# Optimization experiments

Hardware: AMD Instinct MI355X
Metric: run time of the kernel (lower is better)

The kernel has to match this reference:

```python
import jax, jax.numpy as jnp
import numpy as np

NUM_HEADS = 12
EPS = 1e-6


def _rms_norm(x, w):
    # RMSNorm over the full channel dim (applied before head split), fp32 math
    return x * jax.lax.rsqrt(jnp.mean(x * x, axis=-1, keepdims=True) + EPS) * w


def _rope_apply(t, F, H, W, freqs):
    # t: [B, S, n, d] with S == F*H*W; freqs: [1024, d//2] angles
    B, S, n, d = t.shape
    c = d // 2
    s0 = c - 2 * (c // 3)  # temporal split (22 when d=128)
    s1 = c // 3            # spatial splits (21, 21)
    f0, f1, f2 = freqs[:, :s0], freqs[:, s0:s0 + s1], freqs[:, s0 + s1:]
    ang = jnp.concatenate([
        jnp.broadcast_to(f0[:F, None, None, :], (F, H, W, s0)),
        jnp.broadcast_to(f1[None, :H, None, :], (F, H, W, s1)),
        jnp.broadcast_to(f2[None, None, :W, :], (F, H, W, s1)),
    ], axis=-1).reshape(S, c)                      # [S, c]
    cos = jnp.cos(ang)[None, :, None, :]           # [1, S, 1, c]
    sin = jnp.sin(ang)[None, :, None, :]
    tp = t.reshape(B, S, n, c, 2)
    te, to = tp[..., 0], tp[..., 1]                # complex (real, imag) pairs
    rot = jnp.stack([te * cos - to * sin, te * sin + to * cos], axis=-1)
    return rot.reshape(B, S, n, d)


def reference(x, seq_lens, grid_sizes, freqs, Wq, bq, Wk, bk, Wv, bv, Wo, bo, norm_q_w, norm_k_w):
    B, S, C = x.shape
    n = NUM_HEADS
    d = C // n
    gs = np.asarray(grid_sizes)[0]
    F, H, W = int(gs[0]), int(gs[1]), int(gs[2])  # static: L == F*H*W, same per sample

    q = _rms_norm(x @ Wq.T + bq, norm_q_w).reshape(B, S, n, d)
    k = _rms_norm(x @ Wk.T + bk, norm_k_w).reshape(B, S, n, d)
    v = (x @ Wv.T + bv).reshape(B, S, n, d)

    q = _rope_apply(q, F, H, W, freqs)
    k = _rope_apply(k, F, H, W, freqs)

    scale = 1.0 / jnp.sqrt(jnp.float32(d))
    scores = jnp.einsum('bqnd,bknd->bnqk', q, k) * scale   # [B, n, S, S]
    kmask = jnp.arange(S)[None, :] < seq_lens[:, None]      # [B, S] valid keys
    scores = jnp.where(kmask[:, None, None, :], scores, -jnp.inf)
    attn = jax.nn.softmax(scores, axis=-1)
    out = jnp.einsum('bnqk,bknd->bqnd', attn, v).reshape(B, S, C)
    return out @ Wo.T + bo


def setup_inputs() -> dict:
    key = jax.random.key(0)
    ks = jax.random.split(key, 10)
    B, F, H, W = 2, 4, 24, 32
    S = F * H * W  # 3072
    C = 1536
    d = C // NUM_HEADS  # 128
    c = d // 2          # 64

    x = jax.random.normal(ks[0], (B, S, C), dtype=jnp.float32)
    seq_lens = jnp.array([S, 2500], dtype=jnp.int32)
    grid_sizes = jnp.array([[F, H, W]] * B, dtype=jnp.int32)

    # rope angles: outer(pos, 1/theta^(2i/dim)) per split [22, 21, 21]
    def rope_params(max_len, dim_k, theta=10000.0):
        inv = 1.0 / (theta ** (np.arange(0, dim_k, 2, dtype=np.float64) / dim_k))
        return np.outer(np.arange(max_len), inv)
    s0 = c - 2 * (c // 3)
    s1 = c // 3
    freqs = jnp.asarray(np.concatenate([
        rope_params(1024, 2 * s0), rope_params(1024, 2 * s1), rope_params(1024, 2 * s1)
    ], axis=1), dtype=jnp.float32)  # [1024, 64]

    std = 0.02
    def lin(k):
        return jax.random.normal(k, (C, C), dtype=jnp.float32) * std
    return {
        'x': x, 'seq_lens': seq_lens, 'grid_sizes': grid_sizes, 'freqs': freqs,
        'Wq': lin(ks[1]), 'bq': jnp.zeros((C,), jnp.float32),
        'Wk': lin(ks[2]), 'bk': jnp.zeros((C,), jnp.float32),
        'Wv': lin(ks[3]), 'bv': jnp.zeros((C,), jnp.float32),
        'Wo': lin(ks[4]), 'bo': jnp.zeros((C,), jnp.float32),
        'norm_q_w': jnp.ones((C,), jnp.float32),
        'norm_k_w': jnp.ones((C,), jnp.float32),
    }
```

## Files before the change

### kernel.cpp

```cpp
#include <hip/hip_runtime.h>
#include <hip/hip_bf16.h>
#include <math.h>

#define NB 2
#define SS 3072
#define CC 1536
#define NH 12
#define DH 128
#define NTOK (NB * SS)
#define WE (CC * CC)
#define LOG2E 1.4426950408889634f

typedef __attribute__((ext_vector_type(8))) short short8;
typedef __attribute__((ext_vector_type(4))) float floatx4;

#define GLOAD(g, l) __builtin_amdgcn_global_load_lds( \
    (const __attribute__((address_space(1))) void*)(g), \
    (__attribute__((address_space(3))) void*)(l), 16, 0, 0)

__device__ __forceinline__ unsigned short f2bf(float f) {
    unsigned u = __float_as_uint(f);
    u += 0x7fffu + ((u >> 16) & 1u);
    return (unsigned short)(u >> 16);
}
__device__ __forceinline__ int swz(int row, int q) {
    return row * 4 + (q ^ ((row >> 1) & 3));
}

__global__ __launch_bounds__(256) void cast_all(
    const float* __restrict__ x,
    const float* __restrict__ w0, const float* __restrict__ w1,
    const float* __restrict__ w2, const float* __restrict__ w3,
    unsigned short* __restrict__ o)
{
    const int y = blockIdx.y;
    const float* src = (y < 4) ? x + (size_t)y * WE
                     : (y == 4) ? w0 : (y == 5) ? w1 : (y == 6) ? w2 : w3;
    size_t i = ((size_t)blockIdx.x * 256 + threadIdx.x) * 4;
    float4 v = *(const float4*)&src[i];
    uint2 u;
    u.x = (unsigned)f2bf(v.x) | ((unsigned)f2bf(v.y) << 16);
    u.y = (unsigned)f2bf(v.z) | ((unsigned)f2bf(v.w) << 16);
    *(uint2*)&o[(size_t)y * WE + i] = u;
}

__global__ __launch_bounds__(256) void rope_table(
    const float* __restrict__ freqs, const int* __restrict__ gsz,
    float2* __restrict__ tab)
{
    const int id = blockIdx.x * 256 + threadIdx.x;
    const int s = id >> 6, pj = id & 63;
    const int Hg = gsz[1], Wg = gsz[2];
    const int f = s / (Hg * Wg);
    const int rem = s - f * Hg * Wg;
    const int hh = rem / Wg;
    const int ww = rem - hh * Wg;
    const int row = (pj < 22) ? f : ((pj < 43) ? hh : ww);
    float sn, cs;
    sincosf(freqs[row * 64 + pj], &sn, &cs);
    tab[id] = make_float2(cs, sn);
}

__global__ __launch_bounds__(256) void qkv_gemm(
    const unsigned short* __restrict__ X,
    const unsigned short* __restrict__ Wqb, const unsigned short* __restrict__ Wkb,
    const unsigned short* __restrict__ Wvb,
    const float* __restrict__ bq, const float* __restrict__ bk,
    const float* __restrict__ bv,
    unsigned short* __restrict__ qo, unsigned short* __restrict__ ko,
    unsigned short* __restrict__ vto)
{
    __shared__ unsigned short As[128 * 32];
    __shared__ unsigned short Bs[128 * 32];
    const int tid = threadIdx.x;
    const int w = tid >> 6, l = tid & 63;
    const int jseg = blockIdx.y / 12;
    const unsigned short* Wt = (jseg == 0) ? Wqb : (jseg == 1) ? Wkb : Wvb;
    const float* bias        = (jseg == 0) ? bq  : (jseg == 1) ? bk  : bv;
    unsigned short* Y        = (jseg == 0) ? qo  : (jseg == 1) ? ko  : vto;
    const int i0 = blockIdx.x * 128, j0 = (blockIdx.y % 12) * 128;
    const int srow = tid >> 2;
    const int gk8 = (((tid & 3) ^ ((srow >> 1) & 3))) * 8;

    floatx4 acc[4][4] = {};
    for (int k0 = 0; k0 < CC; k0 += 32) {
        __syncthreads();
        GLOAD(X + (size_t)(i0 + srow) * CC + k0 + gk8,        As + (size_t)tid * 8);
        GLOAD(X + (size_t)(i0 + 64 + srow) * CC + k0 + gk8,   As + (size_t)(256 + tid) * 8);
        GLOAD(Wt + (size_t)(j0 + srow) * CC + k0 + gk8,       Bs + (size_t)tid * 8);
        GLOAD(Wt + (size_t)(j0 + 64 + srow) * CC + k0 + gk8,  Bs + (size_t)(256 + tid) * 8);
        __syncthreads();
        const int wr = (w >> 1) * 64, wc = (w & 1) * 64;
        short8 af[4], bf[4];
        #pragma unroll
        for (int mb = 0; mb < 4; ++mb)
            af[mb] = *(const short8*)&As[swz(wr + mb * 16 + (l & 15), l >> 4) * 8];
        #pragma unroll
        for (int nb = 0; nb < 4; ++nb)
            bf[nb] = *(const short8*)&Bs[swz(wc + nb * 16 + (l & 15), l >> 4) * 8];
        #pragma unroll
        for (int mb = 0; mb < 4; ++mb)
            #pragma unroll
            for (int nb = 0; nb < 4; ++nb)
                acc[mb][nb] = __builtin_amdgcn_mfma_f32_16x16x32_bf16(
                    af[mb], bf[nb], acc[mb][nb], 0, 0, 0);
    }

    const int wr = (w >> 1) * 64, wc = (w & 1) * 64;
    #pragma unroll
    for (int mb = 0; mb < 4; ++mb)
        #pragma unroll
        for (int nb = 0; nb < 4; ++nb) {
            const int n = j0 + wc + nb * 16 + (l & 15);
            const float bv2 = bias[n];
            const int h = n >> 7, td = n & 127;
            #pragma unroll
            for (int r = 0; r < 4; ++r) {
                const int m = i0 + wr + mb * 16 + (l >> 4) * 4 + r;
                const float val = acc[mb][nb][r] + bv2;
                const int b = (m >= SS) ? 1 : 0;
                const int s = m - b * SS;
                if (jseg < 2)
                    Y[((size_t)(b * NH + h) * SS + s) * DH + td] = f2bf(val);
                else
                    Y[((size_t)(b * NH + h) * DH + td) * SS + s] = f2bf(val);
            }
        }
}

__global__ __launch_bounds__(256) void gemm_o(
    const unsigned short* __restrict__ X, const unsigned short* __restrict__ Wt,
    const float* __restrict__ bias, float* __restrict__ Y)
{
    __shared__ unsigned short As[128 * 32];
    __shared__ unsigned short Bs[128 * 32];
    const int tid = threadIdx.x;
    const int w = tid >> 6, l = tid & 63;
    const int i0 = blockIdx.x * 128, j0 = blockIdx.y * 128;
    const int srow = tid >> 2;
    const int gk8 = (((tid & 3) ^ ((srow >> 1) & 3))) * 8;

    floatx4 acc[4][4] = {};
    for (int k0 = 0; k0 < CC; k0 += 32) {
        __syncthreads();
        GLOAD(X + (size_t)(i0 + srow) * CC + k0 + gk8,        As + (size_t)tid * 8);
        GLOAD(X + (size_t)(i0 + 64 + srow) * CC + k0 + gk8,   As + (size_t)(256 + tid) * 8);
        GLOAD(Wt + (size_t)(j0 + srow) * CC + k0 + gk8,       Bs + (size_t)tid * 8);
        GLOAD(Wt + (size_t)(j0 + 64 + srow) * CC + k0 + gk8,  Bs + (size_t)(256 + tid) * 8);
        __syncthreads();
        const int wr = (w >> 1) * 64, wc = (w & 1) * 64;
        short8 af[4], bf[4];
        #pragma unroll
        for (int mb = 0; mb < 4; ++mb)
            af[mb] = *(const short8*)&As[swz(wr + mb * 16 + (l & 15), l >> 4) * 8];
        #pragma unroll
        for (int nb = 0; nb < 4; ++nb)
            bf[nb] = *(const short8*)&Bs[swz(wc + nb * 16 + (l & 15), l >> 4) * 8];
        #pragma unroll
        for (int mb = 0; mb < 4; ++mb)
            #pragma unroll
            for (int nb = 0; nb < 4; ++nb)
                acc[mb][nb] = __builtin_amdgcn_mfma_f32_16x16x32_bf16(
                    af[mb], bf[nb], acc[mb][nb], 0, 0, 0);
    }

    const int wr = (w >> 1) * 64, wc = (w & 1) * 64;
    #pragma unroll
    for (int mb = 0; mb < 4; ++mb)
        #pragma unroll
        for (int nb = 0; nb < 4; ++nb) {
            const int n = j0 + wc + nb * 16 + (l & 15);
            const float bv = bias[n];
            #pragma unroll
            for (int r = 0; r < 4; ++r) {
                const int m = i0 + wr + mb * 16 + (l >> 4) * 4 + r;
                Y[(size_t)m * CC + n] = acc[mb][nb][r] + bv;
            }
        }
}

__global__ __launch_bounds__(256) void norm_rope(
    unsigned short* __restrict__ qb, unsigned short* __restrict__ kb,
    const float* __restrict__ nqw, const float* __restrict__ nkw,
    const float2* __restrict__ tab)
{
    const int bid = blockIdx.x;
    const int which = (bid >= NTOK) ? 1 : 0;
    const int tok = bid - which * NTOK;
    unsigned short* t    = which ? kb : qb;
    const float* wgt     = which ? nkw : nqw;
    const float outscale = which ? 1.0f : 0.08838834764831845f * LOG2E;
    const int b = tok / SS, s = tok - b * SS;
    const int tid = threadIdx.x;

    float2 vals[3];
    size_t addrs[3];
    float ss = 0.f;
    #pragma unroll
    for (int kt = 0; kt < 3; ++kt) {
        int p = tid + kt * 256;
        int h = p >> 6, pj = p & 63;
        size_t addr = ((size_t)(b * NH + h) * SS + s) * DH + 2 * pj;
        addrs[kt] = addr;
        unsigned u = *(const unsigned*)&t[addr];
        float2 v;
        v.x = __uint_as_float(u << 16);
        v.y = __uint_as_float(u & 0xffff0000u);
        vals[kt] = v;
        ss += v.x * v.x + v.y * v.y;
    }
    #pragma unroll
    for (int off = 32; off > 0; off >>= 1) ss += __shfl_down(ss, off, 64);
    __shared__ float red[4];
    if ((tid & 63) == 0) red[tid >> 6] = ss;
    __syncthreads();
    const float total = red[0] + red[1] + red[2] + red[3];
    const float rstd = rsqrtf(total * (1.0f / CC) + 1e-6f) * outscale;

    #pragma unroll
    for (int kt = 0; kt < 3; ++kt) {
        int p = tid + kt * 256;
        int h = p >> 6, pj = p & 63;
        float2 cssn = tab[s * 64 + pj];
        int ch = h * DH + 2 * pj;
        float te = vals[kt].x * rstd * wgt[ch];
        float to = vals[kt].y * rstd * wgt[ch + 1];
        unsigned o = (unsigned)f2bf(te * cssn.x - to * cssn.y) |
                     ((unsigned)f2bf(te * cssn.y + to * cssn.x) << 16);
        *(unsigned*)&t[addrs[kt]] = o;
    }
}

__global__ __launch_bounds__(256, 2) void flash_attn_mfma(
    const unsigned short* __restrict__ qg, const unsigned short* __restrict__ kg,
    const unsigned short* __restrict__ vg, const int* __restrict__ seq_lens,
    unsigned short* __restrict__ out)
{
    __shared__ unsigned short lds[32768];
    const int tid = threadIdx.x;
    const int w = tid >> 6, l = tid & 63;

    const int bid = blockIdx.x;
    const int qt = bid / (NB * NH);
    const int rem0 = bid - qt * (NB * NH);
    const int h = rem0 >> 1;
    const int b = rem0 & 1;
    const int slen = seq_lens[b];
    const int s0 = qt * 128;

    const unsigned short* qbase = qg + ((size_t)(b * NH + h) * SS + s0) * DH;
    const unsigned short* kbase = kg + ((size_t)(b * NH + h) * SS) * DH;
    const unsigned short* vbase = vg + ((size_t)(b * NH + h) * DH) * SS;

    #pragma unroll
    for (int i = 0; i < 8; ++i) {
        int cid = i * 256 + tid;
        int kc = cid >> 9, r2 = cid & 511, row = r2 >> 2, sq = r2 & 3;
        GLOAD(qbase + (size_t)row * DH + kc * 32 + (sq ^ ((row >> 1) & 3)) * 8,
              lds + (size_t)cid * 8);
    }
    __syncthreads();
    short8 qf[2][4];
    #pragma unroll
    for (int rb = 0; rb < 2; ++rb)
        #pragma unroll
        for (int kc = 0; kc < 4; ++kc)
            qf[rb][kc] = *(const short8*)&lds[(kc * 512 + swz(w * 32 + rb * 16 + (l & 15), l >> 4)) * 8];
    __syncthreads();

    int ksrc[4], vsrc[4];
    #pragma unroll
    for (int i = 0; i < 4; ++i) {
        int cid = i * 256 + tid;
        {   int kc = cid >> 8, r2 = cid & 255, row = r2 >> 2, sq = r2 & 3;
            ksrc[i] = row * DH + kc * 32 + (sq ^ ((row >> 1) & 3)) * 8; }
        {   int ks = cid >> 9, r2 = cid & 511, dc = r2 >> 2, sq = r2 & 3;
            vsrc[i] = dc * SS + ks * 32 + (sq ^ ((dc >> 1) & 3)) * 8; }
    }

    const int ntiles = (slen + 63) >> 6;

    #pragma unroll
    for (int i = 0; i < 4; ++i) {
        int cid = i * 256 + tid;
        GLOAD(kbase + ksrc[i],        lds + (size_t)cid * 8);
        GLOAD(vbase + vsrc[i],        lds + 8192 + (size_t)cid * 8);
    }

    floatx4 acc[2][8] = {};
    float lsum[2] = {};
    const int g4 = (l >> 4) * 4;

    for (int kt = 0; kt < ntiles; ++kt) {
        __syncthreads();

        if (kt + 1 < ntiles) {
            const unsigned short* kb2 = kbase + (size_t)(kt + 1) * 64 * DH;
            const unsigned short* vb2 = vbase + (size_t)(kt + 1) * 64;
            unsigned short* dst = lds + ((kt + 1) & 1) * 16384;
            #pragma unroll
            for (int i = 0; i < 4; ++i) {
                int cid = i * 256 + tid;
                GLOAD(kb2 + ksrc[i], dst + (size_t)cid * 8);
                GLOAD(vb2 + vsrc[i], dst + 8192 + (size_t)cid * 8);
            }
        }

        const unsigned short* Ks = lds + (kt & 1) * 16384;
        const unsigned short* Vs = Ks + 8192;

        floatx4 sv[2][4] = {};
        __builtin_amdgcn_s_setprio(1);
        #pragma unroll
        for (int kc = 0; kc < 4; ++kc) {
            short8 kf[4];
            #pragma unroll
            for (int nb = 0; nb < 4; ++nb)
                kf[nb] = *(const short8*)&Ks[(kc * 256 + swz(nb * 16 + (l & 15), l >> 4)) * 8];
            #pragma unroll
            for (int rb = 0; rb < 2; ++rb)
                #pragma unroll
                for (int nb = 0; nb < 4; ++nb)
                    sv[rb][nb] = __builtin_amdgcn_mfma_f32_16x16x32_bf16(
                        kf[nb], qf[rb][kc], sv[rb][nb], 0, 0, 0);
        }
        __builtin_amdgcn_s_setprio(0);

        const int valid = slen - kt * 64;
        short8 pa[2][2];
        #pragma unroll
        for (int rb = 0; rb < 2; ++rb) {
            if (valid >= 64) {
                #pragma unroll
                for (int nb = 0; nb < 4; ++nb)
                    #pragma unroll
                    for (int r = 0; r < 4; ++r)
                        sv[rb][nb][r] = exp2f(sv[rb][nb][r]);
            } else {
                #pragma unroll
                for (int nb = 0; nb < 4; ++nb)
                    #pragma unroll
                    for (int r = 0; r < 4; ++r) {
                        const int key = g4 + r + 16 * nb;
                        sv[rb][nb][r] = (key < valid) ? exp2f(sv[rb][nb][r]) : 0.0f;
                    }
            }
            #pragma unroll
            for (int nb = 0; nb < 4; ++nb)
                lsum[rb] += (sv[rb][nb][0] + sv[rb][nb][1]) +
                            (sv[rb][nb][2] + sv[rb][nb][3]);

            unsigned dw0[4], dw1[4];
            #pragma unroll
            for (int nb = 0; nb < 4; ++nb) {
                union { __hip_bfloat162 v; unsigned u; } c0, c1;
                c0.v = __float22bfloat162_rn(make_float2(sv[rb][nb][0], sv[rb][nb][1]));
                c1.v = __float22bfloat162_rn(make_float2(sv[rb][nb][2], sv[rb][nb][3]));
                dw0[nb] = c0.u;
                dw1[nb] = c1.u;
            }
            #pragma unroll
            for (int ks = 0; ks < 2; ++ks) {
                unsigned x0 = dw0[2 * ks], y0 = dw0[2 * ks + 1];
                unsigned x1 = dw1[2 * ks], y1 = dw1[2 * ks + 1];
                asm("v_permlane32_swap_b32 %0, %1" : "+v"(x0), "+v"(y0));
                asm("v_permlane16_swap_b32 %0, %1" : "+v"(x0), "+v"(y0));
                asm("v_permlane32_swap_b32 %0, %1" : "+v"(x1), "+v"(y1));
                asm("v_permlane16_swap_b32 %0, %1" : "+v"(x1), "+v"(y1));
                union { short8 s; unsigned u[4]; } pk;
                pk.u[0] = x0; pk.u[1] = x1; pk.u[2] = y0; pk.u[3] = y1;
                pa[rb][ks] = pk.s;
            }
        }

        __builtin_amdgcn_s_setprio(1);
        #pragma unroll
        for (int ks = 0; ks < 2; ++ks)
            #pragma unroll
            for (int nb2 = 0; nb2 < 8; ++nb2) {
                short8 vf = *(const short8*)&Vs[(ks * 512 + swz(nb2 * 16 + (l & 15), l >> 4)) * 8];
                #pragma unroll
                for (int rb = 0; rb < 2; ++rb)
                    acc[rb][nb2] = __builtin_amdgcn_mfma_f32_16x16x32_bf16(
                        pa[rb][ks], vf, acc[rb][nb2], 0, 0, 0);
            }
        __builtin_amdgcn_s_setprio(0);
    }

    #pragma unroll
    for (int rb = 0; rb < 2; ++rb) {
        float s = lsum[rb];
        s += __shfl_xor(s, 16, 64);
        s += __shfl_xor(s, 32, 64);
        float rl[4];
        #pragma unroll
        for (int r = 0; r < 4; ++r)
            rl[r] = 1.0f / __shfl(s, g4 + r, 64);
        #pragma unroll
        for (int nb2 = 0; nb2 < 8; ++nb2) {
            const int col = h * DH + nb2 * 16 + (l & 15);
            #pragma unroll
            for (int r = 0; r < 4; ++r) {
                const int srow = s0 + w * 32 + rb * 16 + (l >> 4) * 4 + r;
                out[((size_t)b * SS + srow) * CC + col] = f2bf(acc[rb][nb2][r] * rl[r]);
            }
        }
    }
}

extern "C" void kernel_launch(void* const* d_in, const int* in_sizes, int n_in,
                              void* d_out, int out_size, void* d_ws, size_t ws_size,
                              hipStream_t stream) {
    const float* x          = (const float*)d_in[0];
    const int*   seq_lens   = (const int*)d_in[1];
    const int*   grid_sizes = (const int*)d_in[2];
    const float* freqs      = (const float*)d_in[3];
    const float* Wq         = (const float*)d_in[4];
    const float* bq         = (const float*)d_in[5];
    const float* Wk         = (const float*)d_in[6];
    const float* bk         = (const float*)d_in[7];
    const float* Wv         = (const float*)d_in[8];
    const float* bv         = (const float*)d_in[9];
    const float* Wo         = (const float*)d_in[10];
    const float* bo         = (const float*)d_in[11];
    const float* nqw        = (const float*)d_in[12];
    const float* nkw        = (const float*)d_in[13];
    float* out = (float*)d_out;

    const size_t TE = (size_t)NTOK * CC;
    unsigned short* xb  = (unsigned short*)d_ws;
    unsigned short* wqb = xb + TE;
    unsigned short* wkb = wqb + WE;
    unsigned short* wvb = wkb + WE;
    unsigned short* wob = wvb + WE;
    unsigned short* qb  = wob + WE;
    unsigned short* kb  = qb + TE;
    unsigned short* vtb = kb + TE;
    unsigned short* ab  = vtb + TE;
    float2* tab = (float2*)(ab + TE);

    cast_all<<<dim3(WE / 1024, 8), 256, 0, stream>>>(x, Wq, Wk, Wv, Wo, xb);
    rope_table<<<dim3(SS * 64 / 256), 256, 0, stream>>>(freqs, grid_sizes, tab);

    qkv_gemm<<<dim3(NTOK / 128, 36), 256, 0, stream>>>(
        xb, wqb, wkb, wvb, bq, bk, bv, qb, kb, vtb);

    norm_rope<<<dim3(2 * NTOK), 256, 0, stream>>>(qb, kb, nqw, nkw, tab);

    flash_attn_mfma<<<dim3(NB * NH * (SS / 128)), 256, 0, stream>>>(qb, kb, vtb, seq_lens, ab);

    gemm_o<<<dim3(NTOK / 128, CC / 128), 256, 0, stream>>>(ab, wob, bo, out);
}
```

Baseline: 519.1 us.

## Make flash attention persistent with XCD-aware work queues for L2 locality

The attention kernel becomes persistent with 512 blocks. Each block reads its XCD id and pulls work items from one of eight atomic counters, one per XCD. A table assigns (batch, head) combos to XCDs so that all query tiles sharing the same K/V stay on one XCD's L2, and the table mixes long and short sequences to balance load. Blocks steal from other XCD queues when their own is empty. The counters are zeroed inside rope_table, and the scheme adds atomic and barrier overhead per work item.

```diff
diff --git a/kernel.cpp b/kernel.cpp
--- a/kernel.cpp
+++ b/kernel.cpp
@@ -26,6 +26,11 @@
 __device__ __forceinline__ int swz(int row, int q) {
     return row * 4 + (q ^ ((row >> 1) & 3));
 }
+
+__device__ const int comboTab[24] = {
+    0, 16, 9,   2, 18, 11,   4, 20, 13,   6, 22, 15,
+    8, 1, 17,   10, 3, 19,   12, 5, 21,   14, 7, 23
+};
 
 __global__ __launch_bounds__(256) void cast_all(
     const float* __restrict__ x,
@@ -46,9 +51,10 @@
 
 __global__ __launch_bounds__(256) void rope_table(
     const float* __restrict__ freqs, const int* __restrict__ gsz,
-    float2* __restrict__ tab)
+    float2* __restrict__ tab, int* __restrict__ ctr)
 {
     const int id = blockIdx.x * 256 + threadIdx.x;
+    if (id < 8) ctr[id] = 0;
     const int s = id >> 6, pj = id & 63;
     const int Hg = gsz[1], Wg = gsz[2];
     const int f = s / (Hg * Wg);
@@ -234,39 +240,17 @@
 __global__ __launch_bounds__(256, 2) void flash_attn_mfma(
     const unsigned short* __restrict__ qg, const unsigned short* __restrict__ kg,
     const unsigned short* __restrict__ vg, const int* __restrict__ seq_lens,
-    unsigned short* __restrict__ out)
+    unsigned short* __restrict__ out, int* __restrict__ ctr)
 {
     __shared__ unsigned short lds[32768];
+    __shared__ int sw;
     const int tid = threadIdx.x;
     const int w = tid >> 6, l = tid & 63;
-
-    const int bid = blockIdx.x;
-    const int qt = bid / (NB * NH);
-    const int rem0 = bid - qt * (NB * NH);
-    const int h = rem0 >> 1;
-    const int b = rem0 & 1;
-    const int slen = seq_lens[b];
-    const int s0 = qt * 128;
-
-    const unsigned short* qbase = qg + ((size_t)(b * NH + h) * SS + s0) * DH;
-    const unsigned short* kbase = kg + ((size_t)(b * NH + h) * SS) * DH;
-    const unsigned short* vbase = vg + ((size_t)(b * NH + h) * DH) * SS;
-
-    #pragma unroll
-    for (int i = 0; i < 8; ++i) {
-        int cid = i * 256 + tid;
-        int kc = cid >> 9, r2 = cid & 511, row = r2 >> 2, sq = r2 & 3;
-        GLOAD(qbase + (size_t)row * DH + kc * 32 + (sq ^ ((row >> 1) & 3)) * 8,
-              lds + (size_t)cid * 8);
-    }
-    __syncthreads();
-    short8 qf[2][4];
-    #pragma unroll
-    for (int rb = 0; rb < 2; ++rb)
-        #pragma unroll
-        for (int kc = 0; kc < 4; ++kc)
-            qf[rb][kc] = *(const short8*)&lds[(kc * 512 + swz(w * 32 + rb * 16 + (l & 15), l >> 4)) * 8];
-    __syncthreads();
+    const int g4 = (l >> 4) * 4;
+
+    int xcd;
+    asm volatile("s_getreg_b32 %0, hwreg(HW_REG_XCC_ID)" : "=s"(xcd));
+    xcd &= 7;
 
     int ksrc[4], vsrc[4];
     #pragma unroll
@@ -278,131 +262,177 @@
             vsrc[i] = dc * SS + ks * 32 + (sq ^ ((dc >> 1) & 3)) * 8; }
     }
 
-    const int ntiles = (slen + 63) >> 6;
-
-    #pragma unroll
-    for (int i = 0; i < 4; ++i) {
-        int cid = i * 256 + tid;
-        GLOAD(kbase + ksrc[i],        lds + (size_t)cid * 8);
-        GLOAD(vbase + vsrc[i],        lds + 8192 + (size_t)cid * 8);
-    }
-
-    floatx4 acc[2][8] = {};
-    float lsum[2] = {};
-    const int g4 = (l >> 4) * 4;
-
-    for (int kt = 0; kt < ntiles; ++kt) {
-        __syncthreads();
-
-        if (kt + 1 < ntiles) {
-            const unsigned short* kb2 = kbase + (size_t)(kt + 1) * 64 * DH;
-            const unsigned short* vb2 = vbase + (size_t)(kt + 1) * 64;
-            unsigned short* dst = lds + ((kt + 1) & 1) * 16384;
-            #pragma unroll
-            for (int i = 0; i < 4; ++i) {
-                int cid = i * 256 + tid;
-                GLOAD(kb2 + ksrc[i], dst + (size_t)cid * 8);
-                GLOAD(vb2 + vsrc[i], dst + 8192 + (size_t)cid * 8);
-            }
-        }
-
-        const unsigned short* Ks = lds + (kt & 1) * 16384;
-        const unsigned short* Vs = Ks + 8192;
-
-        floatx4 sv[2][4] = {};
-        __builtin_amdgcn_s_setprio(1);
-        #pragma unroll
-        for (int kc = 0; kc < 4; ++kc) {
-            short8 kf[4];
-            #pragma unroll
-            for (int nb = 0; nb < 4; ++nb)
-                kf[nb] = *(const short8*)&Ks[(kc * 256 + swz(nb * 16 + (l & 15), l >> 4)) * 8];
-            #pragma unroll
-            for (int rb = 0; rb < 2; ++rb)
+    for (;;) {
+        __syncthreads();
+        if (tid == 0) {
+            int it = -1;
+            for (int a = 0; a < 8; ++a) {
+                int q = (xcd + a) & 7;
+                int n = atomicAdd(&ctr[q], 1);
+                if (n < 72) {
+                    int c = comboTab[q * 3 + n / 24];
+                    it = c * 24 + (n - (n / 24) * 24);
+                    break;
+                }
+            }
+            sw = it;
+        }
+        __syncthreads();
+        const int item = sw;
+        if (item < 0) break;
+
+        const int c = item / 24;
+        const int qt = item - c * 24;
+        const int h = c >> 1;
+        const int b = c & 1;
+        const int slen = seq_lens[b];
+        const int s0 = qt * 128;
+
+        const unsigned short* qbase = qg + ((size_t)(b * NH + h) * SS + s0) * DH;
+        const unsigned short* kbase = kg + ((size_t)(b * NH + h) * SS) * DH;
+        const unsigned short* vbase = vg + ((size_t)(b * NH + h) * DH) * SS;
+
+        #pragma unroll
+        for (int i = 0; i < 8; ++i) {
+            int cid = i * 256 + tid;
+            int kc = cid >> 9, r2 = cid & 511, row = r2 >> 2, sq = r2 & 3;
+            GLOAD(qbase + (size_t)row * DH + kc * 32 + (sq ^ ((row >> 1) & 3)) * 8,
+                  lds + (size_t)cid * 8);
+        }
+        __syncthreads();
+        short8 qf[2][4];
+        #pragma unroll
+        for (int rb = 0; rb < 2; ++rb)
+            #pragma unroll
+            for (int kc = 0; kc < 4; ++kc)
+                qf[rb][kc] = *(const short8*)&lds[(kc * 512 + swz(w * 32 + rb * 16 + (l & 15), l >> 4)) * 8];
+        __syncthreads();
+
+        const int ntiles = (slen + 63) >> 6;
+
+        #pragma unroll
+        for (int i = 0; i < 4; ++i) {
+            int cid = i * 256 + tid;
+            GLOAD(kbase + ksrc[i],        lds + (size_t)cid * 8);
+            GLOAD(vbase + vsrc[i],        lds + 8192 + (size_t)cid * 8);
+        }
+
+        floatx4 acc[2][8] = {};
+        float lsum[2] = {};
+
+        for (int kt = 0; kt < ntiles; ++kt) {
+            __syncthreads();
+
+            if (kt + 1 < ntiles) {
+                const unsigned short* kb2 = kbase + (size_t)(kt + 1) * 64 * DH;
+                const unsigned short* vb2 = vbase + (size_t)(kt + 1) * 64;
+                unsigned short* dst = lds + ((kt + 1) & 1) * 16384;
+                #pragma unroll
+                for (int i = 0; i < 4; ++i) {
+                    int cid = i * 256 + tid;
+                    GLOAD(kb2 + ksrc[i], dst + (size_t)cid * 8);
+                    GLOAD(vb2 + vsrc[i], dst + 8192 + (size_t)cid * 8);
+                }
+            }
+
+            const unsigned short* Ks = lds + (kt & 1) * 16384;
+            const unsigned short* Vs = Ks + 8192;
+
+            floatx4 sv[2][4] = {};
+            __builtin_amdgcn_s_setprio(1);
+            #pragma unroll
+            for (int kc = 0; kc < 4; ++kc) {
+                short8 kf[4];
                 #pragma unroll
                 for (int nb = 0; nb < 4; ++nb)
-                    sv[rb][nb] = __builtin_amdgcn_mfma_f32_16x16x32_bf16(
-                        kf[nb], qf[rb][kc], sv[rb][nb], 0, 0, 0);
-        }
-        __builtin_amdgcn_s_setprio(0);
-
-        const int valid = slen - kt * 64;
-        short8 pa[2][2];
+                    kf[nb] = *(const short8*)&Ks[(kc * 256 + swz(nb * 16 + (l & 15), l >> 4)) * 8];
+                #pragma unroll
+                for (int rb = 0; rb < 2; ++rb)
+                    #pragma unroll
+                    for (int nb = 0; nb < 4; ++nb)
+                        sv[rb][nb] = __builtin_amdgcn_mfma_f32_16x16x32_bf16(
+                            kf[nb], qf[rb][kc], sv[rb][nb], 0, 0, 0);
+            }
+            __builtin_amdgcn_s_setprio(0);
+
+            const int valid = slen - kt * 64;
+            short8 pa[2][2];
+            #pragma unroll
+            for (int rb = 0; rb < 2; ++rb) {
+                if (valid >= 64) {
+                    #pragma unroll
+                    for (int nb = 0; nb < 4; ++nb)
+                        #pragma unroll
+                        for (int r = 0; r < 4; ++r)
+                            sv[rb][nb][r] = exp2f(sv[rb][nb][r]);
+                } else {
+                    #pragma unroll
+                    for (int nb = 0; nb < 4; ++nb)
+                        #pragma unroll
+                        for (int r = 0; r < 4; ++r) {
+                            const int key = g4 + r + 16 * nb;
+                            sv[rb][nb][r] = (key < valid) ? exp2f(sv[rb][nb][r]) : 0.0f;
+                        }
+                }
+                #pragma unroll
+                for (int nb = 0; nb < 4; ++nb)
+                    lsum[rb] += (sv[rb][nb][0] + sv[rb][nb][1]) +
+                                (sv[rb][nb][2] + sv[rb][nb][3]);
+
+                unsigned dw0[4], dw1[4];
+                #pragma unroll
+                for (int nb = 0; nb < 4; ++nb) {
+                    union { __hip_bfloat162 v; unsigned u; } c0, c1;
+                    c0.v = __float22bfloat162_rn(make_float2(sv[rb][nb][0], sv[rb][nb][1]));
+                    c1.v = __float22bfloat162_rn(make_float2(sv[rb][nb][2], sv[rb][nb][3]));
+                    dw0[nb] = c0.u;
+                    dw1[nb] = c1.u;
+                }
+                #pragma unroll
+                for (int ks = 0; ks < 2; ++ks) {
+                    unsigned x0 = dw0[2 * ks], y0 = dw0[2 * ks + 1];
+                    unsigned x1 = dw1[2 * ks], y1 = dw1[2 * ks + 1];
+                    asm("v_permlane32_swap_b32 %0, %1" : "+v"(x0), "+v"(y0));
+                    asm("v_permlane16_swap_b32 %0, %1" : "+v"(x0), "+v"(y0));
+                    asm("v_permlane32_swap_b32 %0, %1" : "+v"(x1), "+v"(y1));
+                    asm("v_permlane16_swap_b32 %0, %1" : "+v"(x1), "+v"(y1));
+                    union { short8 s; unsigned u[4]; } pk;
+                    pk.u[0] = x0; pk.u[1] = x1; pk.u[2] = y0; pk.u[3] = y1;
+                    pa[rb][ks] = pk.s;
+                }
+            }
+
+            __builtin_amdgcn_s_setprio(1);
+            #pragma unroll
+            for (int ks = 0; ks < 2; ++ks)
+                #pragma unroll
+                for (int nb2 = 0; nb2 < 8; ++nb2) {
+                    short8 vf = *(const short8*)&Vs[(ks * 512 + swz(nb2 * 16 + (l & 15), l >> 4)) * 8];
+                    #pragma unroll
+                    for (int rb = 0; rb < 2; ++rb)
+                        acc[rb][nb2] = __builtin_amdgcn_mfma_f32_16x16x32_bf16(
+                            pa[rb][ks], vf, acc[rb][nb2], 0, 0, 0);
+                }
+            __builtin_amdgcn_s_setprio(0);
+        }
+
         #pragma unroll
         for (int rb = 0; rb < 2; ++rb) {
-            if (valid >= 64) {
-                #pragma unroll
-                for (int nb = 0; nb < 4; ++nb)
-                    #pragma unroll
-                    for (int r = 0; r < 4; ++r)
-                        sv[rb][nb][r] = exp2f(sv[rb][nb][r]);
-            } else {
-                #pragma unroll
-                for (int nb = 0; nb < 4; ++nb)
-                    #pragma unroll
-                    for (int r = 0; r < 4; ++r) {
-                        const int key = g4 + r + 16 * nb;
-                        sv[rb][nb][r] = (key < valid) ? exp2f(sv[rb][nb][r]) : 0.0f;
-                    }
-            }
-            #pragma unroll
-            for (int nb = 0; nb < 4; ++nb)
-                lsum[rb] += (sv[rb][nb][0] + sv[rb][nb][1]) +
-                            (sv[rb][nb][2] + sv[rb][nb][3]);
-
-            unsigned dw0[4], dw1[4];
-            #pragma unroll
-            for (int nb = 0; nb < 4; ++nb) {
-                union { __hip_bfloat162 v; unsigned u; } c0, c1;
-                c0.v = __float22bfloat162_rn(make_float2(sv[rb][nb][0], sv[rb][nb][1]));
-                c1.v = __float22bfloat162_rn(make_float2(sv[rb][nb][2], sv[rb][nb][3]));
-                dw0[nb] = c0.u;
-                dw1[nb] = c1.u;
-            }
-            #pragma unroll
-            for (int ks = 0; ks < 2; ++ks) {
-                unsigned x0 = dw0[2 * ks], y0 = dw0[2 * ks + 1];
-                unsigned x1 = dw1[2 * ks], y1 = dw1[2 * ks + 1];
-                asm("v_permlane32_swap_b32 %0, %1" : "+v"(x0), "+v"(y0));
-                asm("v_permlane16_swap_b32 %0, %1" : "+v"(x0), "+v"(y0));
-                asm("v_permlane32_swap_b32 %0, %1" : "+v"(x1), "+v"(y1));
-                asm("v_permlane16_swap_b32 %0, %1" : "+v"(x1), "+v"(y1));
-                union { short8 s; unsigned u[4]; } pk;
-                pk.u[0] = x0; pk.u[1] = x1; pk.u[2] = y0; pk.u[3] = y1;
-                pa[rb][ks] = pk.s;
-            }
-        }
-
-        __builtin_amdgcn_s_setprio(1);
-        #pragma unroll
-        for (int ks = 0; ks < 2; ++ks)
+            float s = lsum[rb];
+            s += __shfl_xor(s, 16, 64);
+            s += __shfl_xor(s, 32, 64);
+            float rl[4];
+            #pragma unroll
+            for (int r = 0; r < 4; ++r)
+                rl[r] = 1.0f / __shfl(s, g4 + r, 64);
             #pragma unroll
             for (int nb2 = 0; nb2 < 8; ++nb2) {
-                short8 vf = *(const short8*)&Vs[(ks * 512 + swz(nb2 * 16 + (l & 15), l >> 4)) * 8];
-                #pragma unroll
-                for (int rb = 0; rb < 2; ++rb)
-                    acc[rb][nb2] = __builtin_amdgcn_mfma_f32_16x16x32_bf16(
-                        pa[rb][ks], vf, acc[rb][nb2], 0, 0, 0);
-            }
-        __builtin_amdgcn_s_setprio(0);
-    }
-
-    #pragma unroll
-    for (int rb = 0; rb < 2; ++rb) {
-        float s = lsum[rb];
-        s += __shfl_xor(s, 16, 64);
-        s += __shfl_xor(s, 32, 64);
-        float rl[4];
-        #pragma unroll
-        for (int r = 0; r < 4; ++r)
-            rl[r] = 1.0f / __shfl(s, g4 + r, 64);
-        #pragma unroll
-        for (int nb2 = 0; nb2 < 8; ++nb2) {
-            const int col = h * DH + nb2 * 16 + (l & 15);
-            #pragma unroll
-            for (int r = 0; r < 4; ++r) {
-                const int srow = s0 + w * 32 + rb * 16 + (l >> 4) * 4 + r;
-                out[((size_t)b * SS + srow) * CC + col] = f2bf(acc[rb][nb2][r] * rl[r]);
+                const int col = h * DH + nb2 * 16 + (l & 15);
+                #pragma unroll
+                for (int r = 0; r < 4; ++r) {
+                    const int srow = s0 + w * 32 + rb * 16 + (l >> 4) * 4 + r;
+                    out[((size_t)b * SS + srow) * CC + col] = f2bf(acc[rb][nb2][r] * rl[r]);
+                }
             }
         }
     }
@@ -438,16 +468,17 @@
     unsigned short* vtb = kb + TE;
     unsigned short* ab  = vtb + TE;
     float2* tab = (float2*)(ab + TE);
+    int* ctr = (int*)(tab + (size_t)SS * 64);
 
     cast_all<<<dim3(WE / 1024, 8), 256, 0, stream>>>(x, Wq, Wk, Wv, Wo, xb);
-    rope_table<<<dim3(SS * 64 / 256), 256, 0, stream>>>(freqs, grid_sizes, tab);
+    rope_table<<<dim3(SS * 64 / 256), 256, 0, stream>>>(freqs, grid_sizes, tab, ctr);
 
     qkv_gemm<<<dim3(NTOK / 128, 36), 256, 0, stream>>>(
         xb, wqb, wkb, wvb, bq, bk, bv, qb, kb, vtb);
 
     norm_rope<<<dim3(2 * NTOK), 256, 0, stream>>>(qb, kb, nqw, nkw, tab);
 
-    flash_attn_mfma<<<dim3(NB * NH * (SS / 128)), 256, 0, stream>>>(qb, kb, vtb, seq_lens, ab);
+    flash_attn_mfma<<<dim3(512), 256, 0, stream>>>(qb, kb, vtb, seq_lens, ab, ctr);
 
     gemm_o<<<dim3(NTOK / 128, CC / 128), 256, 0, stream>>>(ab, wob, bo, out);
 }
```

Result: slower. 539.5 us (+3.9%).
